# Optimization experiments

Measured on AMD Instinct MI355X. Metric: run time of the kernel, lower is better.

Reference implementation:

```python
import jax, jax.numpy as jnp
import numpy as np

LMAX = 2
C1 = 64; C2 = 64; COUT = 64
B = 4096
SUM_RDIM = sum(3**L for L in range(LMAX + 1))   # 13
FEAT1 = C1 * SUM_RDIM                            # 832
FEAT2 = C2 * SUM_RDIM


def _enumerate_paths(Lmax):
    paths = []
    for L1 in range(Lmax + 1):
        for L2 in range(Lmax + 1):
            for k in range(min(L1, L2) + 1):
                Lout = L1 + L2 - 2 * k
                if 0 <= Lout <= Lmax:
                    paths.append((L1, L2, Lout, k, False))
            if L1 >= 1 and L2 >= 1:
                for k in range(min(L1 - 1, L2 - 1) + 1):
                    Lout = L1 + L2 - 2 * k - 1
                    if 0 <= Lout <= Lmax:
                        paths.append((L1, L2, Lout, k, True))
    return paths

PATHS = _enumerate_paths(LMAX)   # 15 paths for Lmax=2


def _path_eq(L1, L2, k, use_eps):
    # Fused equation: W[c,a,b] contracted together with the delta/eps path einsum.
    letters = list('defghijklmnopqrstuvwxyz')  # a,b,c reserved for channels
    i_idx = letters[:L1]
    j_idx = letters[L1:L1 + L2]
    for r in range(k):  # delta: contract last k indices of A with last k of B
        j_idx[L2 - k + r] = i_idx[L1 - k + r]
    i_free = i_idx[:L1 - k]
    j_free = j_idx[:L2 - k]
    eps_sub = None
    if use_eps:  # consume last free index of each side via eps_{p i j}
        p = letters[L1 + L2]
        eps_sub = p + i_free[-1] + j_free[-1]
        i_free, j_free = i_free[:-1], j_free[:-1]
        out = i_free + j_free + [p]
    else:
        out = i_free + j_free
    terms = ['cab', '...a' + ''.join(i_idx), '...b' + ''.join(j_idx)]
    if eps_sub is not None:
        terms.append(eps_sub)
    return ','.join(terms) + '->...c' + ''.join(out)


def _epsilon():
    e = np.zeros((3, 3, 3), dtype=np.float32)
    e[0, 1, 2] = e[1, 2, 0] = e[2, 0, 1] = 1.0
    e[2, 1, 0] = e[1, 0, 2] = e[0, 2, 1] = -1.0
    return jnp.asarray(e)


def _split_by_rank(x, C, Lmax):
    batch = x.shape[:-1]
    out, idx = {}, 0
    for L in range(Lmax + 1):
        d = C * 3**L
        blk = x[..., idx:idx + d]
        idx += d
        out[L] = blk.reshape(*batch, C) if L == 0 else blk.reshape(*batch, C, *((3,) * L))
    return out


def setup_inputs() -> dict:
    key = jax.random.key(0)
    k1, k2, k3 = jax.random.split(key, 3)
    x1 = jax.random.normal(k1, (B, FEAT1), dtype=jnp.float32)
    x2 = jax.random.normal(k2, (B, FEAT2), dtype=jnp.float32)
    weight = jax.random.normal(k3, (len(PATHS) * COUT * C1 * C2,), dtype=jnp.float32) * 0.02
    return {"x1": x1, "x2": x2, "weight": weight}


def reference(x1, x2, weight):
    A = _split_by_rank(x1, C1, LMAX)
    Bt = _split_by_rank(x2, C2, LMAX)
    eps = _epsilon().astype(x1.dtype)
    batch = x1.shape[:-1]
    blocks = {L: jnp.zeros((*batch, COUT) + (3,) * L, dtype=x1.dtype) for L in range(LMAX + 1)}
    wsz = COUT * C1 * C2
    for n, (L1, L2, Lout, k, use_eps) in enumerate(PATHS):
        Wp = weight[n * wsz:(n + 1) * wsz].reshape(COUT, C1, C2)
        eq = _path_eq(L1, L2, k, use_eps)
        ops = (Wp, A[L1], Bt[L2]) + ((eps,) if use_eps else ())
        blocks[Lout] = blocks[Lout] + jnp.einsum(eq, *ops, optimize='optimal')
    parts = [blocks[L].reshape(*batch, COUT * 3**L) for L in range(LMAX + 1)]
    return jnp.concatenate(parts, axis=-1)
```

## Files before the change

kernel.cpp:

```cpp
#include <hip/hip_runtime.h>
#include <cstdint>
#include <cstddef>


#define FEAT 832
#define ZT 64

typedef _Float16 half8 __attribute__((ext_vector_type(8)));
typedef float floatx16 __attribute__((ext_vector_type(16)));

struct Chunk {
  int wbase;
  int o1[3];
  int o2[3];
  float sg[3];
  int d1, d2, nt;
};

__global__ void swz_w_kernel(const float* __restrict__ w, _Float16* __restrict__ o) {
  const int i = blockIdx.x * 256 + threadIdx.x;
  const int lane = i & 63;
  const int pkc  = i >> 6;
  const int cgrp = pkc & 1;
  const int ksg  = (pkc >> 1) & 255;
  const int p    = pkc >> 9;
  const int c  = cgrp * 32 + (lane & 31);
  const int k0 = ksg * 16 + (lane >> 5) * 8;
  const float* src = w + (size_t)p * 262144 + (size_t)c * 4096 + k0;
  const float4 v0 = *(const float4*)(src);
  const float4 v1 = *(const float4*)(src + 4);
  half8 h = { (_Float16)v0.x, (_Float16)v0.y, (_Float16)v0.z, (_Float16)v0.w,
              (_Float16)v1.x, (_Float16)v1.y, (_Float16)v1.z, (_Float16)v1.w };
  *(half8*)(o + (size_t)i * 8) = h;
}

__device__ __forceinline__ half8 splat8(_Float16 h) {
  return half8{h, h, h, h, h, h, h, h};
}

template<int NT>
__device__ __forceinline__ void run_chunk(
    const Chunk C, const int zbase, const int zl, const int hf,
    const int lane, const int tid, const int a0,
    const float* __restrict__ x1, const float* __restrict__ x2,
    const _Float16* __restrict__ Wh,
    _Float16* __restrict__ XS2, _Float16* __restrict__ XS1,
    floatx16& acc0, floatx16& acc1)
{
  __syncthreads();

  #pragma unroll
  for (int t = 0; t < NT; ++t) {
    const size_t base2 = (size_t)zbase * FEAT + C.o2[t];
    for (int e = tid; e < 4096; e += 256) {
      const int zz = e >> 6, b = e & 63;
      XS2[(t * 64 + zz) * 72 + b] =
          (_Float16)x2[base2 + (size_t)zz * FEAT + b * C.d2];
    }
  }
  #pragma unroll
  for (int t = 0; t < NT; ++t) {
    const float sgf = C.sg[t];
    const int o1 = C.o1[t];
    for (int e = tid; e < 4096; e += 256) {
      const int a = e & 63, zz = e >> 6;
      XS1[(t * 64 + a) * 66 + zz] =
          (_Float16)(x1[(size_t)(zbase + zz) * FEAT + o1 + a * C.d1] * sgf);
    }
  }
  __syncthreads();

  half8 x2r[NT][4];
  #pragma unroll
  for (int t = 0; t < NT; ++t) {
    #pragma unroll
    for (int ks = 0; ks < 4; ++ks)
      x2r[t][ks] = *(const half8*)&XS2[(t * 64 + zl) * 72 + ks * 16 + hf * 8];
  }

  const _Float16* __restrict__ Wq = Wh + C.wbase + lane * 8;
  const _Float16* __restrict__ Xq = XS1 + zl;

  half8 afE[2][4], afO[2][4];
  const _Float16* __restrict__ w0 = Wq + (size_t)a0 * 4096;
  #pragma unroll
  for (int ks = 0; ks < 4; ++ks) {
    afE[0][ks] = *(const half8*)(w0 + ks * 1024);
    afE[1][ks] = *(const half8*)(w0 + ks * 1024 + 512);
    afO[0][ks] = *(const half8*)(w0 + 4096 + ks * 1024);
    afO[1][ks] = *(const half8*)(w0 + 4096 + ks * 1024 + 512);
  }
  _Float16 sc[NT], scn[NT];
  #pragma unroll
  for (int t = 0; t < NT; ++t) {
    sc[t]  = Xq[(t * 64 + a0) * 66];
    scn[t] = Xq[(t * 64 + a0 + 1) * 66];
  }

  const int aend = a0 + 32;
  #pragma unroll 1
  for (int a = a0; a < aend; a += 2) {
    {
      half8 sv[NT];
      #pragma unroll
      for (int t = 0; t < NT; ++t) sv[t] = splat8(sc[t]);
      if (a + 2 < aend) {
        #pragma unroll
        for (int t = 0; t < NT; ++t) sc[t] = Xq[(t * 64 + a + 2) * 66];
      }
      half8 tb = sv[0] * x2r[0][0];
      __builtin_amdgcn_s_setprio(1);
      #pragma unroll
      for (int ks = 0; ks < 4; ++ks) {
        tb = sv[0] * x2r[0][ks];
        if (NT > 1) tb += sv[1] * x2r[1][ks];
        if (NT > 2) tb += sv[2] * x2r[2][ks];
        acc0 = __builtin_amdgcn_mfma_f32_32x32x16_f16(afE[0][ks], tb, acc0, 0, 0, 0);
        acc1 = __builtin_amdgcn_mfma_f32_32x32x16_f16(afE[1][ks], tb, acc1, 0, 0, 0);
      }
      __builtin_amdgcn_s_setprio(0);
      if (a + 2 < aend) {
        const _Float16* wn = Wq + (size_t)(a + 2) * 4096;
        #pragma unroll
        for (int ks = 0; ks < 4; ++ks) {
          afE[0][ks] = *(const half8*)(wn + ks * 1024);
          afE[1][ks] = *(const half8*)(wn + ks * 1024 + 512);
        }
      }
    }
    {
      half8 sv[NT];
      #pragma unroll
      for (int t = 0; t < NT; ++t) sv[t] = splat8(scn[t]);
      if (a + 3 < aend) {
        #pragma unroll
        for (int t = 0; t < NT; ++t) scn[t] = Xq[(t * 64 + a + 3) * 66];
      }
      __builtin_amdgcn_s_setprio(1);
      #pragma unroll
      for (int ks = 0; ks < 4; ++ks) {
        half8 tb = sv[0] * x2r[0][ks];
        if (NT > 1) tb += sv[1] * x2r[1][ks];
        if (NT > 2) tb += sv[2] * x2r[2][ks];
        acc0 = __builtin_amdgcn_mfma_f32_32x32x16_f16(afO[0][ks], tb, acc0, 0, 0, 0);
        acc1 = __builtin_amdgcn_mfma_f32_32x32x16_f16(afO[1][ks], tb, acc1, 0, 0, 0);
      }
      __builtin_amdgcn_s_setprio(0);
      if (a + 3 < aend) {
        const _Float16* wn = Wq + (size_t)(a + 3) * 4096;
        #pragma unroll
        for (int ks = 0; ks < 4; ++ks) {
          afO[0][ks] = *(const half8*)(wn + ks * 1024);
          afO[1][ks] = *(const half8*)(wn + ks * 1024 + 512);
        }
      }
    }
  }
}

__global__ __launch_bounds__(256, 2) void tp_kernel(
    const float* __restrict__ x1, const float* __restrict__ x2,
    const _Float16* __restrict__ Wh, float* __restrict__ out)
{
  __shared__ __align__(16) _Float16 XS2[3 * 64 * 72];
  __shared__ __align__(16) _Float16 XS1[3 * 64 * 66];
  __shared__ Chunk chs[7];
  __shared__ int nch_s;

  const int tid  = threadIdx.x;
  const int slot = blockIdx.y;
  const int zbase = blockIdx.x * ZT;
  const int wid  = tid >> 6;
  const int zgrp = wid & 1;
  const int ah   = wid >> 1;
  const int a0   = ah * 32;
  const int lane = tid & 63;
  const int ln31 = lane & 31;
  const int hf   = lane >> 5;
  const int zl   = zgrp * 32 + ln31;

  int offO, dO, mO;
  if (slot == 0)      { offO = 0;   dO = 1; mO = 0; }
  else if (slot < 4)  { offO = 64;  dO = 3; mO = slot - 1; }
  else                { offO = 256; dO = 9; mO = slot - 4; }

  if (tid == 0) {
    int n = 0;
    auto add = [&](int p, int L1, int L2,
                   int i0, int i1, int i2, int j0, int j1, int j2,
                   float s0, float s1, float s2, int nt) {
      const int offs[3] = {0, 64, 256};
      const int ds[3]   = {1, 3, 9};
      Chunk c;
      c.wbase = p * 262144;
      c.o1[0] = offs[L1] + i0; c.o1[1] = offs[L1] + i1; c.o1[2] = offs[L1] + i2;
      c.o2[0] = offs[L2] + j0; c.o2[1] = offs[L2] + j1; c.o2[2] = offs[L2] + j2;
      c.sg[0] = s0; c.sg[1] = s1; c.sg[2] = s2;
      c.d1 = ds[L1]; c.d2 = ds[L2]; c.nt = nt;
      chs[n++] = c;
    };
    if (slot == 0) {
      add(0, 0,0, 0,0,0, 0,0,0, 1,0,0, 1);
      add(5, 1,1, 0,1,2, 0,1,2, 1,1,1, 3);
      add(13,2,2, 0,1,2, 0,1,2, 1,1,1, 3);
      add(13,2,2, 3,4,5, 3,4,5, 1,1,1, 3);
      add(13,2,2, 6,7,8, 6,7,8, 1,1,1, 3);
    } else if (slot < 4) {
      const int m = slot - 1, p1 = (m+1)%3, p2 = (m+2)%3;
      add(1, 0,1, 0,0,0, m,0,0, 1,0,0, 1);
      add(3, 1,0, m,0,0, 0,0,0, 1,0,0, 1);
      add(6, 1,1, p1,p2,0, p2,p1,0, 1,-1,0, 2);
      add(7, 1,2, 0,1,2, 3*m,3*m+1,3*m+2, 1,1,1, 3);
      add(10,2,1, 3*m,3*m+1,3*m+2, 0,1,2, 1,1,1, 3);
      add(14,2,2, 3*p1,3*p1+1,3*p1+2, 3*p2,3*p2+1,3*p2+2, 1,1,1, 3);
      add(14,2,2, 3*p2,3*p2+1,3*p2+2, 3*p1,3*p1+1,3*p1+2, -1,-1,-1, 3);
    } else {
      const int m = slot - 4, u = m/3, v = m%3, q1 = (v+1)%3, q2 = (v+2)%3;
      add(2, 0,2, 0,0,0, m,0,0, 1,0,0, 1);
      add(4, 1,1, u,0,0, v,0,0, 1,0,0, 1);
      add(8, 1,2, q1,q2,0, 3*u+q2,3*u+q1,0, 1,-1,0, 2);
      add(9, 2,0, m,0,0, 0,0,0, 1,0,0, 1);
      add(11,2,1, 3*u+q1,3*u+q2,0, q2,q1,0, 1,-1,0, 2);
      add(12,2,2, 3*u,3*u+1,3*u+2, 3*v,3*v+1,3*v+2, 1,1,1, 3);
    }
    nch_s = n;
  }
  __syncthreads();
  const int nch = nch_s;

  floatx16 acc0, acc1;
  #pragma unroll
  for (int r = 0; r < 16; ++r) { acc0[r] = 0.0f; acc1[r] = 0.0f; }

  for (int ci = 0; ci < nch; ++ci) {
    const Chunk C = chs[ci];
    if (C.nt == 1)      run_chunk<1>(C, zbase, zl, hf, lane, tid, a0, x1, x2, Wh, XS2, XS1, acc0, acc1);
    else if (C.nt == 2) run_chunk<2>(C, zbase, zl, hf, lane, tid, a0, x1, x2, Wh, XS2, XS1, acc0, acc1);
    else                run_chunk<3>(C, zbase, zl, hf, lane, tid, a0, x1, x2, Wh, XS2, XS1, acc0, acc1);
  }

  __syncthreads();
  float* R = (float*)XS2;
  if (ah == 1) {
    #pragma unroll
    for (int r = 0; r < 16; ++r) {
      R[r * 128 + zgrp * 64 + lane]        = acc0[r];
      R[(16 + r) * 128 + zgrp * 64 + lane] = acc1[r];
    }
  }
  __syncthreads();
  if (ah == 0) {
    #pragma unroll
    for (int r = 0; r < 16; ++r) {
      acc0[r] += R[r * 128 + zgrp * 64 + lane];
      acc1[r] += R[(16 + r) * 128 + zgrp * 64 + lane];
    }

    float* __restrict__ op = out + (size_t)(zbase + zl) * FEAT + offO + mO;
    #pragma unroll
    for (int r = 0; r < 16; ++r) {
      const int cr = (r & 3) + 8 * (r >> 2) + 4 * hf;
      op[(size_t)cr * dO]        = acc0[r];
      op[(size_t)(cr + 32) * dO] = acc1[r];
    }
  }
}

extern "C" void kernel_launch(void* const* d_in, const int* in_sizes, int n_in,
                              void* d_out, int out_size, void* d_ws, size_t ws_size,
                              hipStream_t stream) {
  const float* x1 = (const float*)d_in[0];
  const float* x2 = (const float*)d_in[1];
  const float* w  = (const float*)d_in[2];
  float* out = (float*)d_out;
  _Float16* Wh = (_Float16*)d_ws;

  const int nchunks = 15 * 64 * 4096 / 8;
  hipLaunchKernelGGL(swz_w_kernel, dim3(nchunks / 256), dim3(256), 0, stream, w, Wh);

  dim3 grid(64, 13);
  hipLaunchKernelGGL(tp_kernel, grid, dim3(256), 0, stream, x1, x2, Wh, out);
}
```

Measured before the change: 373.5 us.

## Pre-transpose inputs to fp16 planes and merge output slots into 768-thread blocks

Adds a transpose kernel that converts x1 and x2 into fp16 per-component planes in workspace. The main kernel now loads all 13 x2 planes into LDS once per z-tile and reads x1 scalars straight from global memory, so the per-chunk LDS staging and its barriers go away. Blocks grow to 768 threads and cover three output slots, or split the slot-0 chunks across three wave groups, with a wider LDS reduction at the end. The a-loop is no longer unrolled by two, and signs are applied as fp16 sign-bit XOR. The costs are an extra kernel launch, extra workspace traffic, and lower occupancy from the larger LDS footprint.

```diff
diff --git a/kernel.cpp b/kernel.cpp
--- a/kernel.cpp
+++ b/kernel.cpp
@@ -4,17 +4,16 @@
 
 
 #define FEAT 832
-#define ZT 64
 
 typedef _Float16 half8 __attribute__((ext_vector_type(8)));
 typedef float floatx16 __attribute__((ext_vector_type(16)));
 
 struct Chunk {
   int wbase;
-  int o1[3];
-  int o2[3];
-  float sg[3];
-  int d1, d2, nt;
+  int s1[3];
+  int s2[3];
+  unsigned short sgm[3];
+  int nt;
 };
 
 __global__ void swz_w_kernel(const float* __restrict__ w, _Float16* __restrict__ o) {
@@ -34,6 +33,45 @@
   *(half8*)(o + (size_t)i * 8) = h;
 }
 
+__global__ __launch_bounds__(256) void xpose_kernel(
+    const float* __restrict__ x1, const float* __restrict__ x2,
+    _Float16* __restrict__ X1T, _Float16* __restrict__ X2T)
+{
+  __shared__ _Float16 T[64][66];
+  const int s = blockIdx.y;
+  const int which = blockIdx.z;
+  const int zbase = blockIdx.x * 64;
+  int offs, d, j;
+  if (s == 0)      { offs = 0;   d = 1; j = 0; }
+  else if (s < 4)  { offs = 64;  d = 3; j = s - 1; }
+  else             { offs = 256; d = 9; j = s - 4; }
+  const float* __restrict__ src = which ? x2 : x1;
+  const int tid = threadIdx.x;
+  const int kk = tid & 63;
+  const int z4 = tid >> 6;
+  #pragma unroll
+  for (int i = 0; i < 16; ++i) {
+    const int zz = z4 + i * 4;
+    T[kk][zz] = (_Float16)src[(size_t)(zbase + zz) * FEAT + offs + kk * d + j];
+  }
+  __syncthreads();
+  const int c = tid & 63;
+  const int r4 = tid >> 6;
+  if (which == 0) {
+    #pragma unroll
+    for (int i = 0; i < 16; ++i) {
+      const int a = r4 + i * 4;
+      X1T[(size_t)(s * 64 + a) * 4096 + zbase + c] = T[a][c];
+    }
+  } else {
+    #pragma unroll
+    for (int i = 0; i < 16; ++i) {
+      const int zz = r4 + i * 4;
+      X2T[((size_t)s * 4096 + zbase + zz) * 64 + c] = T[c][zz];
+    }
+  }
+}
+
 __device__ __forceinline__ half8 splat8(_Float16 h) {
   return half8{h, h, h, h, h, h, h, h};
 }
@@ -41,189 +79,164 @@
 template<int NT>
 __device__ __forceinline__ void run_chunk(
     const Chunk C, const int zbase, const int zl, const int hf,
-    const int lane, const int tid, const int a0,
-    const float* __restrict__ x1, const float* __restrict__ x2,
-    const _Float16* __restrict__ Wh,
-    _Float16* __restrict__ XS2, _Float16* __restrict__ XS1,
+    const int lane, const int a0,
+    const _Float16* __restrict__ Wh, const unsigned short* __restrict__ X1u,
+    const _Float16* __restrict__ X2L,
     floatx16& acc0, floatx16& acc1)
 {
-  __syncthreads();
-
+  half8 x2r[NT][4];
   #pragma unroll
   for (int t = 0; t < NT; ++t) {
-    const size_t base2 = (size_t)zbase * FEAT + C.o2[t];
-    for (int e = tid; e < 4096; e += 256) {
-      const int zz = e >> 6, b = e & 63;
-      XS2[(t * 64 + zz) * 72 + b] =
-          (_Float16)x2[base2 + (size_t)zz * FEAT + b * C.d2];
-    }
-  }
+    const _Float16* row = X2L + (C.s2[t] * 64 + zl) * 72 + hf * 8;
+    #pragma unroll
+    for (int ks = 0; ks < 4; ++ks)
+      x2r[t][ks] = *(const half8*)(row + ks * 16);
+  }
+
+  const unsigned short* xp[NT];
+  #pragma unroll
+  for (int t = 0; t < NT; ++t)
+    xp[t] = X1u + (size_t)(C.s1[t] * 64) * 4096 + zbase + zl;
+
+  const _Float16* __restrict__ Wq = Wh + C.wbase + lane * 8;
+
+  half8 af[2][4];
+  {
+    const _Float16* w0 = Wq + (size_t)a0 * 4096;
+    #pragma unroll
+    for (int ks = 0; ks < 4; ++ks) {
+      af[0][ks] = *(const half8*)(w0 + ks * 1024);
+      af[1][ks] = *(const half8*)(w0 + ks * 1024 + 512);
+    }
+  }
+  unsigned short sc[NT], scn[NT];
   #pragma unroll
   for (int t = 0; t < NT; ++t) {
-    const float sgf = C.sg[t];
-    const int o1 = C.o1[t];
-    for (int e = tid; e < 4096; e += 256) {
-      const int a = e & 63, zz = e >> 6;
-      XS1[(t * 64 + a) * 66 + zz] =
-          (_Float16)(x1[(size_t)(zbase + zz) * FEAT + o1 + a * C.d1] * sgf);
-    }
-  }
-  __syncthreads();
-
-  half8 x2r[NT][4];
-  #pragma unroll
-  for (int t = 0; t < NT; ++t) {
-    #pragma unroll
-    for (int ks = 0; ks < 4; ++ks)
-      x2r[t][ks] = *(const half8*)&XS2[(t * 64 + zl) * 72 + ks * 16 + hf * 8];
-  }
-
-  const _Float16* __restrict__ Wq = Wh + C.wbase + lane * 8;
-  const _Float16* __restrict__ Xq = XS1 + zl;
-
-  half8 afE[2][4], afO[2][4];
-  const _Float16* __restrict__ w0 = Wq + (size_t)a0 * 4096;
-  #pragma unroll
-  for (int ks = 0; ks < 4; ++ks) {
-    afE[0][ks] = *(const half8*)(w0 + ks * 1024);
-    afE[1][ks] = *(const half8*)(w0 + ks * 1024 + 512);
-    afO[0][ks] = *(const half8*)(w0 + 4096 + ks * 1024);
-    afO[1][ks] = *(const half8*)(w0 + 4096 + ks * 1024 + 512);
-  }
-  _Float16 sc[NT], scn[NT];
-  #pragma unroll
-  for (int t = 0; t < NT; ++t) {
-    sc[t]  = Xq[(t * 64 + a0) * 66];
-    scn[t] = Xq[(t * 64 + a0 + 1) * 66];
+    sc[t]  = xp[t][(size_t)a0 * 4096];
+    scn[t] = xp[t][(size_t)(a0 + 1) * 4096];
   }
 
   const int aend = a0 + 32;
   #pragma unroll 1
-  for (int a = a0; a < aend; a += 2) {
-    {
-      half8 sv[NT];
+  for (int a = a0; a < aend; ++a) {
+    half8 sv[NT];
+    #pragma unroll
+    for (int t = 0; t < NT; ++t) {
+      unsigned short u = (unsigned short)(sc[t] ^ C.sgm[t]);
+      _Float16 h;
+      __builtin_memcpy(&h, &u, 2);
+      sv[t] = splat8(h);
+    }
+    #pragma unroll
+    for (int t = 0; t < NT; ++t) sc[t] = scn[t];
+    if (a + 2 < aend) {
       #pragma unroll
-      for (int t = 0; t < NT; ++t) sv[t] = splat8(sc[t]);
-      if (a + 2 < aend) {
-        #pragma unroll
-        for (int t = 0; t < NT; ++t) sc[t] = Xq[(t * 64 + a + 2) * 66];
-      }
-      half8 tb = sv[0] * x2r[0][0];
-      __builtin_amdgcn_s_setprio(1);
+      for (int t = 0; t < NT; ++t) scn[t] = xp[t][(size_t)(a + 2) * 4096];
+    }
+    __builtin_amdgcn_s_setprio(1);
+    #pragma unroll
+    for (int ks = 0; ks < 4; ++ks) {
+      half8 tb = sv[0] * x2r[0][ks];
+      if (NT > 1) tb += sv[1] * x2r[1][ks];
+      if (NT > 2) tb += sv[2] * x2r[2][ks];
+      acc0 = __builtin_amdgcn_mfma_f32_32x32x16_f16(af[0][ks], tb, acc0, 0, 0, 0);
+      acc1 = __builtin_amdgcn_mfma_f32_32x32x16_f16(af[1][ks], tb, acc1, 0, 0, 0);
+    }
+    __builtin_amdgcn_s_setprio(0);
+    if (a + 1 < aend) {
+      const _Float16* wn = Wq + (size_t)(a + 1) * 4096;
       #pragma unroll
       for (int ks = 0; ks < 4; ++ks) {
-        tb = sv[0] * x2r[0][ks];
-        if (NT > 1) tb += sv[1] * x2r[1][ks];
-        if (NT > 2) tb += sv[2] * x2r[2][ks];
-        acc0 = __builtin_amdgcn_mfma_f32_32x32x16_f16(afE[0][ks], tb, acc0, 0, 0, 0);
-        acc1 = __builtin_amdgcn_mfma_f32_32x32x16_f16(afE[1][ks], tb, acc1, 0, 0, 0);
+        af[0][ks] = *(const half8*)(wn + ks * 1024);
+        af[1][ks] = *(const half8*)(wn + ks * 1024 + 512);
       }
-      __builtin_amdgcn_s_setprio(0);
-      if (a + 2 < aend) {
-        const _Float16* wn = Wq + (size_t)(a + 2) * 4096;
-        #pragma unroll
-        for (int ks = 0; ks < 4; ++ks) {
-          afE[0][ks] = *(const half8*)(wn + ks * 1024);
-          afE[1][ks] = *(const half8*)(wn + ks * 1024 + 512);
-        }
-      }
-    }
-    {
-      half8 sv[NT];
-      #pragma unroll
-      for (int t = 0; t < NT; ++t) sv[t] = splat8(scn[t]);
-      if (a + 3 < aend) {
-        #pragma unroll
-        for (int t = 0; t < NT; ++t) scn[t] = Xq[(t * 64 + a + 3) * 66];
-      }
-      __builtin_amdgcn_s_setprio(1);
-      #pragma unroll
-      for (int ks = 0; ks < 4; ++ks) {
-        half8 tb = sv[0] * x2r[0][ks];
-        if (NT > 1) tb += sv[1] * x2r[1][ks];
-        if (NT > 2) tb += sv[2] * x2r[2][ks];
-        acc0 = __builtin_amdgcn_mfma_f32_32x32x16_f16(afO[0][ks], tb, acc0, 0, 0, 0);
-        acc1 = __builtin_amdgcn_mfma_f32_32x32x16_f16(afO[1][ks], tb, acc1, 0, 0, 0);
-      }
-      __builtin_amdgcn_s_setprio(0);
-      if (a + 3 < aend) {
-        const _Float16* wn = Wq + (size_t)(a + 3) * 4096;
-        #pragma unroll
-        for (int ks = 0; ks < 4; ++ks) {
-          afO[0][ks] = *(const half8*)(wn + ks * 1024);
-          afO[1][ks] = *(const half8*)(wn + ks * 1024 + 512);
-        }
-      }
-    }
-  }
-}
-
-__global__ __launch_bounds__(256, 2) void tp_kernel(
-    const float* __restrict__ x1, const float* __restrict__ x2,
-    const _Float16* __restrict__ Wh, float* __restrict__ out)
+    }
+  }
+}
+
+__global__ __launch_bounds__(768) void tp_kernel(
+    const _Float16* __restrict__ Wh, const unsigned short* __restrict__ X1u,
+    const _Float16* __restrict__ X2Tg, float* __restrict__ out)
 {
-  __shared__ __align__(16) _Float16 XS2[3 * 64 * 72];
-  __shared__ __align__(16) _Float16 XS1[3 * 64 * 66];
-  __shared__ Chunk chs[7];
+  __shared__ __align__(16) _Float16 X2L[13 * 64 * 72];
+  __shared__ Chunk chs[3][7];
   __shared__ int nch_s;
 
-  const int tid  = threadIdx.x;
-  const int slot = blockIdx.y;
-  const int zbase = blockIdx.x * ZT;
+  const int tid = threadIdx.x;
+  const int bid = blockIdx.x;
+  int g, zt;
+  if (bid < 256) { const int u = (bid & 7) * 32 + (bid >> 3); g = 1 + (u >> 6); zt = u & 63; }
+  else           { g = 0; zt = bid - 256; }
+  const int zbase = zt * 64;
   const int wid  = tid >> 6;
-  const int zgrp = wid & 1;
-  const int ah   = wid >> 1;
-  const int a0   = ah * 32;
+  const int zg   = wid & 1;
+  const int aq   = (wid >> 1) & 1;
+  const int mm   = wid >> 2;
+  const int a0   = aq * 32;
   const int lane = tid & 63;
   const int ln31 = lane & 31;
   const int hf   = lane >> 5;
-  const int zl   = zgrp * 32 + ln31;
-
-  int offO, dO, mO;
-  if (slot == 0)      { offO = 0;   dO = 1; mO = 0; }
-  else if (slot < 4)  { offO = 64;  dO = 3; mO = slot - 1; }
-  else                { offO = 256; dO = 9; mO = slot - 4; }
+  const int zl   = zg * 32 + ln31;
 
   if (tid == 0) {
-    int n = 0;
-    auto add = [&](int p, int L1, int L2,
-                   int i0, int i1, int i2, int j0, int j1, int j2,
-                   float s0, float s1, float s2, int nt) {
-      const int offs[3] = {0, 64, 256};
-      const int ds[3]   = {1, 3, 9};
-      Chunk c;
-      c.wbase = p * 262144;
-      c.o1[0] = offs[L1] + i0; c.o1[1] = offs[L1] + i1; c.o1[2] = offs[L1] + i2;
-      c.o2[0] = offs[L2] + j0; c.o2[1] = offs[L2] + j1; c.o2[2] = offs[L2] + j2;
-      c.sg[0] = s0; c.sg[1] = s1; c.sg[2] = s2;
-      c.d1 = ds[L1]; c.d2 = ds[L2]; c.nt = nt;
-      chs[n++] = c;
-    };
-    if (slot == 0) {
-      add(0, 0,0, 0,0,0, 0,0,0, 1,0,0, 1);
-      add(5, 1,1, 0,1,2, 0,1,2, 1,1,1, 3);
-      add(13,2,2, 0,1,2, 0,1,2, 1,1,1, 3);
-      add(13,2,2, 3,4,5, 3,4,5, 1,1,1, 3);
-      add(13,2,2, 6,7,8, 6,7,8, 1,1,1, 3);
-    } else if (slot < 4) {
-      const int m = slot - 1, p1 = (m+1)%3, p2 = (m+2)%3;
-      add(1, 0,1, 0,0,0, m,0,0, 1,0,0, 1);
-      add(3, 1,0, m,0,0, 0,0,0, 1,0,0, 1);
-      add(6, 1,1, p1,p2,0, p2,p1,0, 1,-1,0, 2);
-      add(7, 1,2, 0,1,2, 3*m,3*m+1,3*m+2, 1,1,1, 3);
-      add(10,2,1, 3*m,3*m+1,3*m+2, 0,1,2, 1,1,1, 3);
-      add(14,2,2, 3*p1,3*p1+1,3*p1+2, 3*p2,3*p2+1,3*p2+2, 1,1,1, 3);
-      add(14,2,2, 3*p2,3*p2+1,3*p2+2, 3*p1,3*p1+1,3*p1+2, -1,-1,-1, 3);
-    } else {
-      const int m = slot - 4, u = m/3, v = m%3, q1 = (v+1)%3, q2 = (v+2)%3;
-      add(2, 0,2, 0,0,0, m,0,0, 1,0,0, 1);
-      add(4, 1,1, u,0,0, v,0,0, 1,0,0, 1);
-      add(8, 1,2, q1,q2,0, 3*u+q2,3*u+q1,0, 1,-1,0, 2);
-      add(9, 2,0, m,0,0, 0,0,0, 1,0,0, 1);
-      add(11,2,1, 3*u+q1,3*u+q2,0, q2,q1,0, 1,-1,0, 2);
-      add(12,2,2, 3*u,3*u+1,3*u+2, 3*v,3*v+1,3*v+2, 1,1,1, 3);
-    }
-    nch_s = n;
+    auto plane = [](int L, int j) { return L == 0 ? 0 : (L == 1 ? 1 + j : 4 + j); };
+    for (int m = 0; m < 3; ++m) {
+      int n = 0;
+      auto add = [&](int p, int L1, int L2, int i0,int i1,int i2,
+                     int j0,int j1,int j2, float s0,float s1,float s2, int nt) {
+        Chunk c;
+        c.wbase = p * 262144;
+        const int is[3] = {i0,i1,i2}, js[3] = {j0,j1,j2};
+        const float ss[3] = {s0,s1,s2};
+        for (int t = 0; t < 3; ++t) {
+          c.s1[t] = plane(L1, is[t]);
+          c.s2[t] = plane(L2, js[t]);
+          c.sgm[t] = ss[t] < 0.f ? (unsigned short)0x8000 : (unsigned short)0;
+        }
+        c.nt = nt;
+        chs[m][n++] = c;
+      };
+      if (g == 0) {
+        if (m == 0) {
+          add(0, 0,0, 0,0,0, 0,0,0, 1,0,0, 1);
+          add(5, 1,1, 0,1,2, 0,1,2, 1,1,1, 3);
+          add(13,2,2, 0,1,2, 0,1,2, 1,1,1, 3);
+          add(13,2,2, 3,4,5, 3,4,5, 1,1,1, 3);
+          add(13,2,2, 6,7,8, 6,7,8, 1,1,1, 3);
+          nch_s = n;
+        }
+      } else {
+        const int slot = 3 * g - 2 + m;
+        if (slot < 4) {
+          const int mi = slot - 1, p1 = (mi+1)%3, p2 = (mi+2)%3;
+          add(1, 0,1, 0,0,0, mi,0,0, 1,0,0, 1);
+          add(3, 1,0, mi,0,0, 0,0,0, 1,0,0, 1);
+          add(6, 1,1, p1,p2,0, p2,p1,0, 1,-1,0, 2);
+          add(7, 1,2, 0,1,2, 3*mi,3*mi+1,3*mi+2, 1,1,1, 3);
+          add(10,2,1, 3*mi,3*mi+1,3*mi+2, 0,1,2, 1,1,1, 3);
+          add(14,2,2, 3*p1,3*p1+1,3*p1+2, 3*p2,3*p2+1,3*p2+2, 1,1,1, 3);
+          add(14,2,2, 3*p2,3*p2+1,3*p2+2, 3*p1,3*p1+1,3*p1+2, -1,-1,-1, 3);
+        } else {
+          const int mi = slot - 4, uu = mi/3, v = mi%3, q1 = (v+1)%3, q2 = (v+2)%3;
+          add(2, 0,2, 0,0,0, mi,0,0, 1,0,0, 1);
+          add(4, 1,1, uu,0,0, v,0,0, 1,0,0, 1);
+          add(8, 1,2, q1,q2,0, 3*uu+q2,3*uu+q1,0, 1,-1,0, 2);
+          add(9, 2,0, mi,0,0, 0,0,0, 1,0,0, 1);
+          add(11,2,1, 3*uu+q1,3*uu+q2,0, q2,q1,0, 1,-1,0, 2);
+          add(12,2,2, 3*uu,3*uu+1,3*uu+2, 3*v,3*v+1,3*v+2, 1,1,1, 3);
+        }
+        nch_s = n;
+      }
+    }
+  }
+
+  for (int idx = tid; idx < 13 * 64 * 8; idx += 768) {
+    const int s  = idx >> 9;
+    const int rem = idx & 511;
+    const int zz = rem >> 3;
+    const int o8 = rem & 7;
+    *(half8*)(X2L + (s * 64 + zz) * 72 + o8 * 8) =
+        *(const half8*)(X2Tg + ((size_t)s * 4096 + zbase + zz) * 64 + o8 * 8);
   }
   __syncthreads();
   const int nch = nch_s;
@@ -232,30 +245,62 @@
   #pragma unroll
   for (int r = 0; r < 16; ++r) { acc0[r] = 0.0f; acc1[r] = 0.0f; }
 
-  for (int ci = 0; ci < nch; ++ci) {
-    const Chunk C = chs[ci];
-    if (C.nt == 1)      run_chunk<1>(C, zbase, zl, hf, lane, tid, a0, x1, x2, Wh, XS2, XS1, acc0, acc1);
-    else if (C.nt == 2) run_chunk<2>(C, zbase, zl, hf, lane, tid, a0, x1, x2, Wh, XS2, XS1, acc0, acc1);
-    else                run_chunk<3>(C, zbase, zl, hf, lane, tid, a0, x1, x2, Wh, XS2, XS1, acc0, acc1);
+  if (g == 0) {
+    for (int ci = mm; ci < nch; ci += 3) {
+      const Chunk C = chs[0][ci];
+      if (C.nt == 1)      run_chunk<1>(C, zbase, zl, hf, lane, a0, Wh, X1u, X2L, acc0, acc1);
+      else if (C.nt == 2) run_chunk<2>(C, zbase, zl, hf, lane, a0, Wh, X1u, X2L, acc0, acc1);
+      else                run_chunk<3>(C, zbase, zl, hf, lane, a0, Wh, X1u, X2L, acc0, acc1);
+    }
+  } else {
+    for (int ci = 0; ci < nch; ++ci) {
+      const Chunk C = chs[mm][ci];
+      if (C.nt == 1)      run_chunk<1>(C, zbase, zl, hf, lane, a0, Wh, X1u, X2L, acc0, acc1);
+      else if (C.nt == 2) run_chunk<2>(C, zbase, zl, hf, lane, a0, Wh, X1u, X2L, acc0, acc1);
+      else                run_chunk<3>(C, zbase, zl, hf, lane, a0, Wh, X1u, X2L, acc0, acc1);
+    }
   }
 
   __syncthreads();
-  float* R = (float*)XS2;
-  if (ah == 1) {
+  float* __restrict__ Dv = (float*)X2L;
+  const bool writer = (aq == 0) && (g > 0 || mm == 0);
+  if (!writer) {
+    const int b = ((mm * 2 + aq) * 2 + zg) * 2048;
     #pragma unroll
     for (int r = 0; r < 16; ++r) {
-      R[r * 128 + zgrp * 64 + lane]        = acc0[r];
-      R[(16 + r) * 128 + zgrp * 64 + lane] = acc1[r];
+      Dv[b + r * 64 + lane]        = acc0[r];
+      Dv[b + 1024 + r * 64 + lane] = acc1[r];
     }
   }
   __syncthreads();
-  if (ah == 0) {
-    #pragma unroll
-    for (int r = 0; r < 16; ++r) {
-      acc0[r] += R[r * 128 + zgrp * 64 + lane];
-      acc1[r] += R[(16 + r) * 128 + zgrp * 64 + lane];
-    }
-
+  if (writer) {
+    if (g > 0) {
+      const int b = ((mm * 2 + 1) * 2 + zg) * 2048;
+      #pragma unroll
+      for (int r = 0; r < 16; ++r) {
+        acc0[r] += Dv[b + r * 64 + lane];
+        acc1[r] += Dv[b + 1024 + r * 64 + lane];
+      }
+    } else {
+      #pragma unroll
+      for (int m2 = 0; m2 < 3; ++m2) {
+        #pragma unroll
+        for (int q2 = 0; q2 < 2; ++q2) {
+          if (m2 == 0 && q2 == 0) continue;
+          const int b = ((m2 * 2 + q2) * 2 + zg) * 2048;
+          #pragma unroll
+          for (int r = 0; r < 16; ++r) {
+            acc0[r] += Dv[b + r * 64 + lane];
+            acc1[r] += Dv[b + 1024 + r * 64 + lane];
+          }
+        }
+      }
+    }
+    const int slot = (g == 0) ? 0 : 3 * g - 2 + mm;
+    int offO, dO, mO;
+    if (slot == 0)      { offO = 0;   dO = 1; mO = 0; }
+    else if (slot < 4)  { offO = 64;  dO = 3; mO = slot - 1; }
+    else                { offO = 256; dO = 9; mO = slot - 4; }
     float* __restrict__ op = out + (size_t)(zbase + zl) * FEAT + offO + mO;
     #pragma unroll
     for (int r = 0; r < 16; ++r) {
@@ -273,11 +318,14 @@
   const float* x2 = (const float*)d_in[1];
   const float* w  = (const float*)d_in[2];
   float* out = (float*)d_out;
-  _Float16* Wh = (_Float16*)d_ws;
+  _Float16* Wh  = (_Float16*)d_ws;
+  _Float16* X1T = (_Float16*)((char*)d_ws + 7864320);
+  _Float16* X2T = (_Float16*)((char*)d_ws + 7864320 + 6815744);
 
   const int nchunks = 15 * 64 * 4096 / 8;
   hipLaunchKernelGGL(swz_w_kernel, dim3(nchunks / 256), dim3(256), 0, stream, w, Wh);
-
-  dim3 grid(64, 13);
-  hipLaunchKernelGGL(tp_kernel, grid, dim3(256), 0, stream, x1, x2, Wh, out);
-}
+  hipLaunchKernelGGL(xpose_kernel, dim3(64, 13, 2), dim3(256), 0, stream,
+                     x1, x2, X1T, X2T);
+  hipLaunchKernelGGL(tp_kernel, dim3(320), dim3(768), 0, stream,
+                     Wh, (const unsigned short*)X1T, X2T, out);
+}
```

New measurement: 464.1 us. +24.3%, slower.
